# Kernel optimization log

Measured on AMD Instinct MI355X. Metric: run time of the kernel, lower is better.

The kernel has to match this reference:

```python
import jax, jax.numpy as jnp
import numpy as np

MAX_LENGTH = 30
SOS_TOKEN = 2
V, E, H = 32000, 512, 512
B, S = 64, 128


def setup_inputs() -> dict:
    key = jax.random.key(0)
    ks = jax.random.split(key, 16)
    sc = 0.02
    return {
        "encoder_outputs": jax.random.normal(ks[0], (B, S, 2 * H), jnp.float32),
        "encoder_hidden": jax.random.normal(ks[1], (B, H), jnp.float32),
        "target_tensor": jax.random.randint(ks[2], (B, MAX_LENGTH), 0, V, jnp.int32),
        "embedding": jax.random.normal(ks[3], (V, E), jnp.float32) * sc,
        "wa": jax.random.normal(ks[4], (H, H), jnp.float32) * sc,
        "ua": jax.random.normal(ks[5], (H, 2 * H), jnp.float32) * sc,
        "va": jax.random.normal(ks[6], (1, H), jnp.float32) * sc,
        "w_ih": jax.random.normal(ks[7], (3 * H, E + 2 * H), jnp.float32) * sc,
        "w_hh": jax.random.normal(ks[8], (3 * H, H), jnp.float32) * sc,
        "b_ih": jnp.zeros((3 * H,), jnp.float32),
        "b_hh": jnp.zeros((3 * H,), jnp.float32),
        "fc_w": jax.random.normal(ks[9], (V, E + 3 * H), jnp.float32) * sc,
        "fc_b": jnp.zeros((V,), jnp.float32),
    }


def reference(encoder_outputs, encoder_hidden, target_tensor, embedding, wa, ua, va,
              w_ih, w_hh, b_ih, b_hh, fc_w, fc_b):
    b = encoder_outputs.shape[0]
    # teacher-forced input tokens per step: SOS then target[:, :-1]  -> [T, B]
    toks = jnp.concatenate(
        [jnp.full((b, 1), SOS_TOKEN, target_tensor.dtype), target_tensor[:, :-1]], axis=1).T
    enc_ua = jnp.einsum('bsk,hk->bsh', encoder_outputs, ua)  # precompute ua(enc)

    def step(hidden, tok):
        emb = embedding[tok]                                   # [B, E] (dropout = eval mode)
        # Bahdanau attention
        energy = jnp.tanh(hidden @ wa.T[None][0][None][0] if False else jnp.tanh(0))  # placeholder
        energy = jnp.tanh((hidden @ wa.T)[:, None, :] + enc_ua)  # [B, S, H]
        scores = jnp.einsum('bsh,h->bs', energy, va[0])          # [B, S]
        attw = jax.nn.softmax(scores, axis=-1)
        context = jnp.einsum('bs,bsd->bd', attw, encoder_outputs)  # [B, 2H]
        # GRU cell (PyTorch gate order: r, z, n)
        x = jnp.concatenate([emb, context], axis=-1)             # [B, E+2H]
        gi = x @ w_ih.T + b_ih
        gh = hidden @ w_hh.T + b_hh
        i_r, i_z, i_n = jnp.split(gi, 3, axis=-1)
        h_r, h_z, h_n = jnp.split(gh, 3, axis=-1)
        r = jax.nn.sigmoid(i_r + h_r)
        z = jax.nn.sigmoid(i_z + h_z)
        n = jnp.tanh(i_n + r * h_n)
        h_new = (1.0 - z) * n + z * hidden
        out = jnp.concatenate([emb, h_new, context], axis=-1) @ fc_w.T + fc_b  # [B, V]
        return h_new, out

    _, outs = jax.lax.scan(step, encoder_hidden, toks)  # outs: [T, B, V]
    logits = jnp.transpose(outs, (1, 0, 2))             # [B, T, V]
    return jax.nn.log_softmax(logits, axis=-1)
```

## Files before the change

### kernel.cpp

```cpp
#include <hip/hip_runtime.h>

#define B_ 64
#define S_ 128
#define H_ 512
#define E_ 512
#define V_ 32000
#define T_ 30
#define KX_ 1536
#define KF_ 2048

typedef float f32x4 __attribute__((ext_vector_type(4)));
typedef short s16x8 __attribute__((ext_vector_type(8)));
typedef short s16x4 __attribute__((ext_vector_type(4)));

__device__ __forceinline__ short f2bf(float f) {
  union { float f; unsigned u; } v; v.f = f;
  unsigned r = v.u + 0x7fffu + ((v.u >> 16) & 1u);
  return (short)(r >> 16);
}
__device__ __forceinline__ float bf2f(short s) {
  union { unsigned u; float f; } v; v.u = ((unsigned)(unsigned short)s) << 16;
  return v.f;
}

__device__ __forceinline__ f32x4 mfma16(s16x8 a, s16x8 b, f32x4 c) {
  return __builtin_amdgcn_mfma_f32_16x16x32_bf16(a, b, c, 0, 0, 0);
}

__global__ __launch_bounds__(256) void cvt_bf16_kernel(const float* __restrict__ src,
                                                       short* __restrict__ dst, int n4) {
  int i = blockIdx.x * 256 + threadIdx.x;
  if (i >= n4) return;
  f32x4 v = *(const f32x4*)(src + (size_t)i * 4);
  s16x4 o;
  o[0] = f2bf(v[0]); o[1] = f2bf(v[1]); o[2] = f2bf(v[2]); o[3] = f2bf(v[3]);
  *(s16x4*)(dst + (size_t)i * 4) = o;
}

__global__ __launch_bounds__(256) void init_kernel(const float* __restrict__ ehid,
                                                   float* __restrict__ hidden,
                                                   short* __restrict__ xg) {
  int i = blockIdx.x * 256 + threadIdx.x;
  float h = ehid[i];
  hidden[i] = h;
  int b = i >> 9, hh = i & 511;
  xg[b * 2048 + 1536 + hh] = f2bf(h);
}

__global__ __launch_bounds__(256) void enc_ua_kernel(const float* __restrict__ enc,
                                                     const float* __restrict__ ua,
                                                     short* __restrict__ enc_ua) {
  __shared__ short alds[64 * 264];
  int tid = threadIdx.x;
  int wv = tid >> 6, lane = tid & 63;
  int q = lane >> 4, ml = lane & 15;
  int m0 = blockIdx.x * 64;
  int n0 = blockIdx.y * 128 + wv * 32;
  f32x4 acc[4][2];
  f32x4 zz = {0.f, 0.f, 0.f, 0.f};
#pragma unroll
  for (int a = 0; a < 4; a++) { acc[a][0] = zz; acc[a][1] = zz; }

  for (int kc = 0; kc < 4; kc++) {
    __syncthreads();
    for (int i = tid; i < 4096; i += 256) {
      int m = i >> 6, kk = (i & 63) << 2;
      f32x4 v = *(const f32x4*)(enc + (size_t)(m0 + m) * 1024 + kc * 256 + kk);
      s16x4 o;
      o[0] = f2bf(v[0]); o[1] = f2bf(v[1]); o[2] = f2bf(v[2]); o[3] = f2bf(v[3]);
      *(s16x4*)(&alds[m * 264 + kk]) = o;
    }
    __syncthreads();
#pragma unroll
    for (int kt = 0; kt < 8; kt++) {
      int k = kt * 32 + q * 8;
      int gk = kc * 256 + k;
      s16x8 bf[2];
#pragma unroll
      for (int nf = 0; nf < 2; nf++) {
        const float* bp = ua + (size_t)(n0 + nf * 16 + ml) * 1024 + gk;
        f32x4 b0 = *(const f32x4*)bp, b1 = *(const f32x4*)(bp + 4);
        s16x8 t;
        t[0] = f2bf(b0[0]); t[1] = f2bf(b0[1]); t[2] = f2bf(b0[2]); t[3] = f2bf(b0[3]);
        t[4] = f2bf(b1[0]); t[5] = f2bf(b1[1]); t[6] = f2bf(b1[2]); t[7] = f2bf(b1[3]);
        bf[nf] = t;
      }
#pragma unroll
      for (int mt = 0; mt < 4; mt++) {
        s16x8 af = *(const s16x8*)(&alds[(mt * 16 + ml) * 264 + k]);
        acc[mt][0] = mfma16(af, bf[0], acc[mt][0]);
        acc[mt][1] = mfma16(af, bf[1], acc[mt][1]);
      }
    }
  }
#pragma unroll
  for (int nf = 0; nf < 2; nf++) {
    int n = n0 + nf * 16 + ml;
#pragma unroll
    for (int mt = 0; mt < 4; mt++)
#pragma unroll
      for (int r = 0; r < 4; r++) {
        int m = m0 + mt * 16 + q * 4 + r;
        enc_ua[(size_t)m * 512 + n] = f2bf(acc[mt][nf][r]);
      }
  }
}

__global__ __launch_bounds__(256) void prep_kernel(const short* __restrict__ xg_h,
                                                   const short* __restrict__ wab,
                                                   float* __restrict__ qv,
                                                   const float* __restrict__ embedding,
                                                   const int* __restrict__ target,
                                                   short* __restrict__ xg,
                                                   short* __restrict__ xf, int t) {
  int tid = threadIdx.x;
  int wv = tid >> 6, lane = tid & 63;
  int q = lane >> 4, ml = lane & 15;
  int n = blockIdx.x * 64 + wv * 16 + ml;
  f32x4 acc[4];
  f32x4 zz = {0.f, 0.f, 0.f, 0.f};
#pragma unroll
  for (int a = 0; a < 4; a++) acc[a] = zz;

#pragma unroll
  for (int kt = 0; kt < 16; kt++) {
    int k = kt * 32 + q * 8;
    s16x8 bfrag = *(const s16x8*)(wab + (size_t)n * 512 + k);
#pragma unroll
    for (int mt = 0; mt < 4; mt++) {
      s16x8 af = *(const s16x8*)(xg_h + (size_t)(mt * 16 + ml) * 2048 + 1536 + k);
      acc[mt] = mfma16(af, bfrag, acc[mt]);
    }
  }
#pragma unroll
  for (int mt = 0; mt < 4; mt++)
#pragma unroll
    for (int r = 0; r < 4; r++) {
      int b = mt * 16 + q * 4 + r;
      qv[(size_t)b * 512 + n] = acc[mt][r];
    }

  int gid = blockIdx.x * 256 + tid;
#pragma unroll
  for (int it = 0; it < 16; it++) {
    int i = gid + it * 2048;
    int b = i >> 9, h = i & 511;
    int tok = (t == 0) ? 2 : target[b * 30 + (t - 1)];
    short s = f2bf(embedding[(size_t)tok * 512 + h]);
    xg[b * 2048 + h] = s;
    xf[b * 2048 + h] = s;
  }
}

__global__ __launch_bounds__(256) void score_kernel(const float* __restrict__ qv,
                                                    const float* __restrict__ va,
                                                    const short* __restrict__ enc_ua,
                                                    float* __restrict__ scores) {
  int b = blockIdx.x >> 3;
  int sg = blockIdx.x & 7;
  int tid = threadIdx.x;
  int wv = tid >> 6, lane = tid & 63;
  __shared__ float qv_s[512];
  __shared__ float va_s[512];
  for (int i = tid; i < 512; i += 256) {
    qv_s[i] = qv[b * 512 + i];
    va_s[i] = va[i];
  }
  __syncthreads();
#pragma unroll
  for (int r = 0; r < 4; r++) {
    int s = sg * 16 + wv * 4 + r;
    const short* eu = enc_ua + ((size_t)b * 128 + s) * 512 + lane * 8;
    s16x8 e8 = *(const s16x8*)eu;
    float a = 0.f;
#pragma unroll
    for (int j = 0; j < 8; j++) {
      int h = lane * 8 + j;
      float e = qv_s[h] + bf2f(e8[j]);
      float ex = __expf(2.f * e);
      float th = 1.f - 2.f / (ex + 1.f);
      a += th * va_s[h];
    }
#pragma unroll
    for (int off = 32; off > 0; off >>= 1) a += __shfl_down(a, off);
    if (lane == 0) scores[b * 128 + s] = a;
  }
}

template <bool ENCB>
__global__ __launch_bounds__(256) void ctx_kernel(const float* __restrict__ scores,
                                                  const float* __restrict__ encf,
                                                  const short* __restrict__ encb,
                                                  short* __restrict__ xg,
                                                  short* __restrict__ xf) {
  int b = blockIdx.x, tid = threadIdx.x;
  __shared__ float p[128];
  __shared__ float red[128];
  if (tid < 128) { p[tid] = scores[b * 128 + tid]; red[tid] = p[tid]; }
  __syncthreads();
  for (int st = 64; st >= 1; st >>= 1) {
    if (tid < st) red[tid] = fmaxf(red[tid], red[tid + st]);
    __syncthreads();
  }
  float mx = red[0];
  __syncthreads();
  if (tid < 128) { float e = __expf(p[tid] - mx); p[tid] = e; red[tid] = e; }
  __syncthreads();
  for (int st = 64; st >= 1; st >>= 1) {
    if (tid < st) red[tid] += red[tid + st];
    __syncthreads();
  }
  float inv = 1.f / red[0];
  __syncthreads();
  if (tid < 128) p[tid] *= inv;
  __syncthreads();

  int d = blockIdx.y * 256 + tid;
  float a = 0.f;
  if (ENCB) {
    const short* ep = encb + (size_t)b * 128 * 1024 + d;
#pragma unroll 4
    for (int s = 0; s < 128; s++) a += p[s] * bf2f(ep[(size_t)s * 1024]);
  } else {
    const float* ep = encf + (size_t)b * 128 * 1024 + d;
#pragma unroll 4
    for (int s = 0; s < 128; s++) a += p[s] * ep[(size_t)s * 1024];
  }
  short c = f2bf(a);
  xg[b * 2048 + 512 + d] = c;
  xf[b * 2048 + 1024 + d] = c;
}

__global__ __launch_bounds__(256) void gru_gemm_kernel(const short* __restrict__ xg,
                                                       const short* __restrict__ wihb,
                                                       const short* __restrict__ whhb,
                                                       float* __restrict__ gi,
                                                       float* __restrict__ gh) {
  int tid = threadIdx.x;
  int wv = tid >> 6, lane = tid & 63;
  int q = lane >> 4, ml = lane & 15;
  int n = blockIdx.x * 64 + wv * 16 + ml;
  f32x4 acci[4], acch[4];
  f32x4 zz = {0.f, 0.f, 0.f, 0.f};
#pragma unroll
  for (int a = 0; a < 4; a++) { acci[a] = zz; acch[a] = zz; }

  for (int kt = 0; kt < 48; kt++) {
    int k = kt * 32 + q * 8;
    s16x8 bfrag = *(const s16x8*)(wihb + (size_t)n * 1536 + k);
#pragma unroll
    for (int mt = 0; mt < 4; mt++) {
      s16x8 af = *(const s16x8*)(xg + (size_t)(mt * 16 + ml) * 2048 + k);
      acci[mt] = mfma16(af, bfrag, acci[mt]);
    }
  }
  for (int kt = 0; kt < 16; kt++) {
    int k = kt * 32 + q * 8;
    s16x8 bfrag = *(const s16x8*)(whhb + (size_t)n * 512 + k);
#pragma unroll
    for (int mt = 0; mt < 4; mt++) {
      s16x8 af = *(const s16x8*)(xg + (size_t)(mt * 16 + ml) * 2048 + 1536 + k);
      acch[mt] = mfma16(af, bfrag, acch[mt]);
    }
  }
#pragma unroll
  for (int mt = 0; mt < 4; mt++)
#pragma unroll
    for (int r = 0; r < 4; r++) {
      int b = mt * 16 + q * 4 + r;
      gi[(size_t)b * 1536 + n] = acci[mt][r];
      gh[(size_t)b * 1536 + n] = acch[mt][r];
    }
}

__global__ __launch_bounds__(256) void gates_kernel(const float* __restrict__ gi,
                                                    const float* __restrict__ gh,
                                                    const float* __restrict__ bih,
                                                    const float* __restrict__ bhh,
                                                    float* __restrict__ hidden,
                                                    short* __restrict__ xg,
                                                    short* __restrict__ xf) {
  int i = blockIdx.x * 256 + threadIdx.x;
  int b = i >> 9, h = i & 511;
  const float* gib = gi + (size_t)b * 1536;
  const float* ghb = gh + (size_t)b * 1536;
  float ir = gib[h] + bih[h];
  float iz = gib[512 + h] + bih[512 + h];
  float in_ = gib[1024 + h] + bih[1024 + h];
  float hr = ghb[h] + bhh[h];
  float hz = ghb[512 + h] + bhh[512 + h];
  float hn = ghb[1024 + h] + bhh[1024 + h];
  float r = 1.f / (1.f + __expf(-(ir + hr)));
  float z = 1.f / (1.f + __expf(-(iz + hz)));
  float nx = in_ + r * hn;
  float ex = __expf(2.f * nx);
  float n = 1.f - 2.f / (ex + 1.f);
  float hnew = (1.f - z) * n + z * hidden[i];
  hidden[i] = hnew;
  short hb = f2bf(hnew);
  xg[b * 2048 + 1536 + h] = hb;
  xf[b * 2048 + 512 + h] = hb;
}

template <bool PRE>
__global__ __launch_bounds__(256) void fc_kernel(const short* __restrict__ xf,
                                                 const short* __restrict__ fcwb,
                                                 const float* __restrict__ fcwf,
                                                 const float* __restrict__ fcb,
                                                 float* __restrict__ out, int t) {
  __shared__ short alds[64 * 264];
  int tid = threadIdx.x;
  int wv = tid >> 6, lane = tid & 63;
  int q = lane >> 4, ml = lane & 15;
  int n0 = blockIdx.x * 128 + wv * 32;
  f32x4 acc[4][2];
  f32x4 zz = {0.f, 0.f, 0.f, 0.f};
#pragma unroll
  for (int a = 0; a < 4; a++) { acc[a][0] = zz; acc[a][1] = zz; }

  for (int kc = 0; kc < 8; kc++) {
    __syncthreads();
    for (int i = tid; i < 2048; i += 256) {
      int m = i >> 5, kk = (i & 31) << 3;
      *(s16x8*)(&alds[m * 264 + kk]) = *(const s16x8*)(xf + (size_t)m * 2048 + kc * 256 + kk);
    }
    __syncthreads();
#pragma unroll
    for (int kt = 0; kt < 8; kt++) {
      int k = kt * 32 + q * 8;
      int gk = kc * 256 + k;
      s16x8 bf0, bf1;
      if (PRE) {
        bf0 = *(const s16x8*)(fcwb + (size_t)(n0 + ml) * 2048 + gk);
        bf1 = *(const s16x8*)(fcwb + (size_t)(n0 + 16 + ml) * 2048 + gk);
      } else {
        const float* p0 = fcwf + (size_t)(n0 + ml) * 2048 + gk;
        const float* p1 = fcwf + (size_t)(n0 + 16 + ml) * 2048 + gk;
        f32x4 a0 = *(const f32x4*)p0, a1 = *(const f32x4*)(p0 + 4);
        f32x4 b0 = *(const f32x4*)p1, b1 = *(const f32x4*)(p1 + 4);
        bf0[0] = f2bf(a0[0]); bf0[1] = f2bf(a0[1]); bf0[2] = f2bf(a0[2]); bf0[3] = f2bf(a0[3]);
        bf0[4] = f2bf(a1[0]); bf0[5] = f2bf(a1[1]); bf0[6] = f2bf(a1[2]); bf0[7] = f2bf(a1[3]);
        bf1[0] = f2bf(b0[0]); bf1[1] = f2bf(b0[1]); bf1[2] = f2bf(b0[2]); bf1[3] = f2bf(b0[3]);
        bf1[4] = f2bf(b1[0]); bf1[5] = f2bf(b1[1]); bf1[6] = f2bf(b1[2]); bf1[7] = f2bf(b1[3]);
      }
#pragma unroll
      for (int mt = 0; mt < 4; mt++) {
        s16x8 af = *(const s16x8*)(&alds[(mt * 16 + ml) * 264 + k]);
        acc[mt][0] = mfma16(af, bf0, acc[mt][0]);
        acc[mt][1] = mfma16(af, bf1, acc[mt][1]);
      }
    }
  }
#pragma unroll
  for (int nf = 0; nf < 2; nf++) {
    int v = n0 + nf * 16 + ml;
    float bias = fcb[v];
#pragma unroll
    for (int mt = 0; mt < 4; mt++)
#pragma unroll
      for (int r = 0; r < 4; r++) {
        int b = mt * 16 + q * 4 + r;
        out[((size_t)b * T_ + t) * V_ + v] = acc[mt][nf][r] + bias;
      }
  }
}

__global__ __launch_bounds__(256) void finalize_kernel(float* __restrict__ out, int t) {
  int b = blockIdx.x, tid = threadIdx.x;
  float* row = out + ((size_t)b * T_ + t) * V_;
  __shared__ float red[256];
  float mx = -3.4e38f;
  for (int i = tid; i < 8000; i += 256) {
    f32x4 v = *(const f32x4*)(row + i * 4);
    mx = fmaxf(mx, fmaxf(fmaxf(v[0], v[1]), fmaxf(v[2], v[3])));
  }
  red[tid] = mx; __syncthreads();
  for (int st = 128; st >= 1; st >>= 1) {
    if (tid < st) red[tid] = fmaxf(red[tid], red[tid + st]);
    __syncthreads();
  }
  mx = red[0]; __syncthreads();
  float sm = 0.f;
  for (int i = tid; i < 8000; i += 256) {
    f32x4 v = *(const f32x4*)(row + i * 4);
    sm += __expf(v[0] - mx) + __expf(v[1] - mx) + __expf(v[2] - mx) + __expf(v[3] - mx);
  }
  red[tid] = sm; __syncthreads();
  for (int st = 128; st >= 1; st >>= 1) {
    if (tid < st) red[tid] += red[tid + st];
    __syncthreads();
  }
  float lse = mx + __logf(red[0]);
  for (int i = tid; i < 8000; i += 256) {
    f32x4 v = *(const f32x4*)(row + i * 4);
    v[0] -= lse; v[1] -= lse; v[2] -= lse; v[3] -= lse;
    *(f32x4*)(row + i * 4) = v;
  }
}

extern "C" void kernel_launch(void* const* d_in, const int* in_sizes, int n_in,
                              void* d_out, int out_size, void* d_ws, size_t ws_size,
                              hipStream_t stream) {
  const float* enc  = (const float*)d_in[0];
  const float* ehid = (const float*)d_in[1];
  const int*   tgt  = (const int*)  d_in[2];
  const float* emb  = (const float*)d_in[3];
  const float* wa   = (const float*)d_in[4];
  const float* ua   = (const float*)d_in[5];
  const float* va   = (const float*)d_in[6];
  const float* wih  = (const float*)d_in[7];
  const float* whh  = (const float*)d_in[8];
  const float* bih  = (const float*)d_in[9];
  const float* bhh  = (const float*)d_in[10];
  const float* fcw  = (const float*)d_in[11];
  const float* fcb  = (const float*)d_in[12];
  float* out = (float*)d_out;

  const size_t SZ_FCWB = (size_t)V_ * KF_ * 2;
  const size_t SZ_ENCB = (size_t)B_ * S_ * 1024 * 2;
  char* ws = (char*)d_ws;
  size_t off = 0;
  auto take = [&](size_t bytes) -> char* {
    char* p = ws + off;
    off = (off + bytes + 255) & ~(size_t)255;
    return p;
  };
  size_t small_need;
  {
    size_t o = 0;
    auto sim = [&](size_t bb) { o = (o + bb + 255) & ~(size_t)255; };
    sim((size_t)B_ * S_ * H_ * 2);
    sim((size_t)3 * H_ * KX_ * 2);
    sim((size_t)3 * H_ * H_ * 2);
    sim((size_t)H_ * H_ * 2);
    sim((size_t)B_ * H_ * 4);
    sim((size_t)B_ * H_ * 4);
    sim((size_t)B_ * S_ * 4);
    sim((size_t)B_ * KF_ * 2);
    sim((size_t)B_ * KF_ * 2);
    sim((size_t)B_ * 3 * H_ * 4);
    sim((size_t)B_ * 3 * H_ * 4);
    small_need = o;
  }
  bool PRE  = ws_size >= SZ_FCWB + small_need + 512;
  bool ENCB = ws_size >= SZ_FCWB + SZ_ENCB + small_need + 1024;

  short* fcwb = PRE ? (short*)take(SZ_FCWB) : nullptr;
  short* encb = ENCB ? (short*)take(SZ_ENCB) : nullptr;
  short* enc_ua = (short*)take((size_t)B_ * S_ * H_ * 2);
  short* wihb   = (short*)take((size_t)3 * H_ * KX_ * 2);
  short* whhb   = (short*)take((size_t)3 * H_ * H_ * 2);
  short* wab    = (short*)take((size_t)H_ * H_ * 2);
  float* hidden = (float*)take((size_t)B_ * H_ * 4);
  float* qv     = (float*)take((size_t)B_ * H_ * 4);
  float* scores = (float*)take((size_t)B_ * S_ * 4);
  short* xg     = (short*)take((size_t)B_ * KF_ * 2);
  short* xf     = (short*)take((size_t)B_ * KF_ * 2);
  float* gi     = (float*)take((size_t)B_ * 3 * H_ * 4);
  float* gh     = (float*)take((size_t)B_ * 3 * H_ * 4);

  if (PRE)
    cvt_bf16_kernel<<<(V_ * KF_ / 4 + 255) / 256, 256, 0, stream>>>(fcw, fcwb, V_ * KF_ / 4);
  if (ENCB)
    cvt_bf16_kernel<<<(B_ * S_ * 1024 / 4 + 255) / 256, 256, 0, stream>>>(enc, encb, B_ * S_ * 1024 / 4);
  cvt_bf16_kernel<<<(3 * H_ * KX_ / 4 + 255) / 256, 256, 0, stream>>>(wih, wihb, 3 * H_ * KX_ / 4);
  cvt_bf16_kernel<<<(3 * H_ * H_ / 4 + 255) / 256, 256, 0, stream>>>(whh, whhb, 3 * H_ * H_ / 4);
  cvt_bf16_kernel<<<(H_ * H_ / 4 + 255) / 256, 256, 0, stream>>>(wa, wab, H_ * H_ / 4);
  init_kernel<<<(B_ * H_) / 256, 256, 0, stream>>>(ehid, hidden, xg);
  enc_ua_kernel<<<dim3(128, 4), 256, 0, stream>>>(enc, ua, enc_ua);

  for (int t = 0; t < T_; t++) {
    prep_kernel<<<8, 256, 0, stream>>>(xg, wab, qv, emb, tgt, xg, xf, t);
    score_kernel<<<B_ * 8, 256, 0, stream>>>(qv, va, enc_ua, scores);
    if (ENCB)
      ctx_kernel<true><<<dim3(B_, 4), 256, 0, stream>>>(scores, enc, encb, xg, xf);
    else
      ctx_kernel<false><<<dim3(B_, 4), 256, 0, stream>>>(scores, enc, encb, xg, xf);
    gru_gemm_kernel<<<24, 256, 0, stream>>>(xg, wihb, whhb, gi, gh);
    gates_kernel<<<(B_ * H_) / 256, 256, 0, stream>>>(gi, gh, bih, bhh, hidden, xg, xf);
    if (PRE)
      fc_kernel<true><<<V_ / 128, 256, 0, stream>>>(xf, fcwb, fcw, fcb, out, t);
    else
      fc_kernel<false><<<V_ / 128, 256, 0, stream>>>(xf, fcwb, fcw, fcb, out, t);
    finalize_kernel<<<B_, 256, 0, stream>>>(out, t);
  }
}
```

Baseline: 4.705 ms.

## Replace per-step kernel launches with a persistent decoder kernel using grid barriers

```diff
diff --git a/kernel.cpp b/kernel.cpp
--- a/kernel.cpp
+++ b/kernel.cpp
@@ -22,9 +22,19 @@
   union { unsigned u; float f; } v; v.u = ((unsigned)(unsigned short)s) << 16;
   return v.f;
 }
-
 __device__ __forceinline__ f32x4 mfma16(s16x8 a, s16x8 b, f32x4 c) {
   return __builtin_amdgcn_mfma_f32_16x16x32_bf16(a, b, c, 0, 0, 0);
+}
+
+__device__ __forceinline__ void gbar(unsigned* cnt, unsigned target) {
+  __threadfence();
+  __syncthreads();
+  if (threadIdx.x == 0) {
+    atomicAdd(cnt, 1u);
+    while (atomicAdd(cnt, 0u) < target) __builtin_amdgcn_s_sleep(1);
+  }
+  __syncthreads();
+  __threadfence();
 }
 
 __global__ __launch_bounds__(256) void cvt_bf16_kernel(const float* __restrict__ src,
@@ -39,8 +49,10 @@
 
 __global__ __launch_bounds__(256) void init_kernel(const float* __restrict__ ehid,
                                                    float* __restrict__ hidden,
-                                                   short* __restrict__ xg) {
+                                                   short* __restrict__ xg,
+                                                   unsigned* __restrict__ bar) {
   int i = blockIdx.x * 256 + threadIdx.x;
+  if (blockIdx.x == 0 && threadIdx.x < 64) bar[threadIdx.x] = 0u;
   float h = ehid[i];
   hidden[i] = h;
   int b = i >> 9, hh = i & 511;
@@ -80,10 +92,10 @@
       for (int nf = 0; nf < 2; nf++) {
         const float* bp = ua + (size_t)(n0 + nf * 16 + ml) * 1024 + gk;
         f32x4 b0 = *(const f32x4*)bp, b1 = *(const f32x4*)(bp + 4);
-        s16x8 t;
-        t[0] = f2bf(b0[0]); t[1] = f2bf(b0[1]); t[2] = f2bf(b0[2]); t[3] = f2bf(b0[3]);
-        t[4] = f2bf(b1[0]); t[5] = f2bf(b1[1]); t[6] = f2bf(b1[2]); t[7] = f2bf(b1[3]);
-        bf[nf] = t;
+        s16x8 tt;
+        tt[0] = f2bf(b0[0]); tt[1] = f2bf(b0[1]); tt[2] = f2bf(b0[2]); tt[3] = f2bf(b0[3]);
+        tt[4] = f2bf(b1[0]); tt[5] = f2bf(b1[1]); tt[6] = f2bf(b1[2]); tt[7] = f2bf(b1[3]);
+        bf[nf] = tt;
       }
 #pragma unroll
       for (int mt = 0; mt < 4; mt++) {
@@ -106,272 +118,83 @@
   }
 }
 
-__global__ __launch_bounds__(256) void prep_kernel(const short* __restrict__ xg_h,
-                                                   const short* __restrict__ wab,
-                                                   float* __restrict__ qv,
-                                                   const float* __restrict__ embedding,
-                                                   const int* __restrict__ target,
-                                                   short* __restrict__ xg,
-                                                   short* __restrict__ xf, int t) {
-  int tid = threadIdx.x;
-  int wv = tid >> 6, lane = tid & 63;
-  int q = lane >> 4, ml = lane & 15;
-  int n = blockIdx.x * 64 + wv * 16 + ml;
+__global__ __launch_bounds__(256) void emb_gather_kernel(const float* __restrict__ emb,
+                                                         const int* __restrict__ tgt,
+                                                         short* __restrict__ emb_all) {
+  int b = blockIdx.x, t = blockIdx.y, tid = threadIdx.x;
+  int tok = (t == 0) ? 2 : tgt[b * 30 + (t - 1)];
+  const float* src = emb + (size_t)tok * 512;
+  short* dst = emb_all + ((size_t)t * 64 + b) * 512;
+  int h = tid * 2;
+  float a0 = src[h], a1 = src[h + 1];
+  dst[h] = f2bf(a0); dst[h + 1] = f2bf(a1);
+}
+
+struct PP {
+  const short* fcwb; const float* fcwf; const float* fcb;
+  const short* encb; const float* encf;
+  const short* enc_ua; const short* wab;
+  const short* wihb; const short* whhb;
+  const float* bih; const float* bhh; const float* va;
+  const short* emb_all;
+  short* xg0; short* xg1; short* xf0; short* xf1;
+  float* hid0; float* hid1; float* qv; float* out;
+  unsigned* bar;
+};
+
+template <bool PRE>
+static __device__ void fc_tile(int tile, int tf, const short* __restrict__ xfb,
+                               const PP& P, float* smf) {
+  short* alds = (short*)smf;
+  const int tid = threadIdx.x;
+  const int wv = tid >> 6, lane = tid & 63;
+  const int q = lane >> 4, ml = lane & 15;
+  const int n = tile * 64 + wv * 16 + ml;
+  const f32x4 zz = {0.f, 0.f, 0.f, 0.f};
   f32x4 acc[4];
-  f32x4 zz = {0.f, 0.f, 0.f, 0.f};
-#pragma unroll
-  for (int a = 0; a < 4; a++) acc[a] = zz;
-
-#pragma unroll
-  for (int kt = 0; kt < 16; kt++) {
-    int k = kt * 32 + q * 8;
-    s16x8 bfrag = *(const s16x8*)(wab + (size_t)n * 512 + k);
-#pragma unroll
-    for (int mt = 0; mt < 4; mt++) {
-      s16x8 af = *(const s16x8*)(xg_h + (size_t)(mt * 16 + ml) * 2048 + 1536 + k);
-      acc[mt] = mfma16(af, bfrag, acc[mt]);
-    }
-  }
-#pragma unroll
-  for (int mt = 0; mt < 4; mt++)
-#pragma unroll
-    for (int r = 0; r < 4; r++) {
-      int b = mt * 16 + q * 4 + r;
-      qv[(size_t)b * 512 + n] = acc[mt][r];
-    }
-
-  int gid = blockIdx.x * 256 + tid;
-#pragma unroll
-  for (int it = 0; it < 16; it++) {
-    int i = gid + it * 2048;
-    int b = i >> 9, h = i & 511;
-    int tok = (t == 0) ? 2 : target[b * 30 + (t - 1)];
-    short s = f2bf(embedding[(size_t)tok * 512 + h]);
-    xg[b * 2048 + h] = s;
-    xf[b * 2048 + h] = s;
-  }
-}
-
-__global__ __launch_bounds__(256) void score_kernel(const float* __restrict__ qv,
-                                                    const float* __restrict__ va,
-                                                    const short* __restrict__ enc_ua,
-                                                    float* __restrict__ scores) {
-  int b = blockIdx.x >> 3;
-  int sg = blockIdx.x & 7;
-  int tid = threadIdx.x;
-  int wv = tid >> 6, lane = tid & 63;
-  __shared__ float qv_s[512];
-  __shared__ float va_s[512];
-  for (int i = tid; i < 512; i += 256) {
-    qv_s[i] = qv[b * 512 + i];
-    va_s[i] = va[i];
-  }
-  __syncthreads();
-#pragma unroll
-  for (int r = 0; r < 4; r++) {
-    int s = sg * 16 + wv * 4 + r;
-    const short* eu = enc_ua + ((size_t)b * 128 + s) * 512 + lane * 8;
-    s16x8 e8 = *(const s16x8*)eu;
-    float a = 0.f;
-#pragma unroll
-    for (int j = 0; j < 8; j++) {
-      int h = lane * 8 + j;
-      float e = qv_s[h] + bf2f(e8[j]);
-      float ex = __expf(2.f * e);
-      float th = 1.f - 2.f / (ex + 1.f);
-      a += th * va_s[h];
-    }
-#pragma unroll
-    for (int off = 32; off > 0; off >>= 1) a += __shfl_down(a, off);
-    if (lane == 0) scores[b * 128 + s] = a;
-  }
-}
-
-template <bool ENCB>
-__global__ __launch_bounds__(256) void ctx_kernel(const float* __restrict__ scores,
-                                                  const float* __restrict__ encf,
-                                                  const short* __restrict__ encb,
-                                                  short* __restrict__ xg,
-                                                  short* __restrict__ xf) {
-  int b = blockIdx.x, tid = threadIdx.x;
-  __shared__ float p[128];
-  __shared__ float red[128];
-  if (tid < 128) { p[tid] = scores[b * 128 + tid]; red[tid] = p[tid]; }
-  __syncthreads();
-  for (int st = 64; st >= 1; st >>= 1) {
-    if (tid < st) red[tid] = fmaxf(red[tid], red[tid + st]);
-    __syncthreads();
-  }
-  float mx = red[0];
-  __syncthreads();
-  if (tid < 128) { float e = __expf(p[tid] - mx); p[tid] = e; red[tid] = e; }
-  __syncthreads();
-  for (int st = 64; st >= 1; st >>= 1) {
-    if (tid < st) red[tid] += red[tid + st];
-    __syncthreads();
-  }
-  float inv = 1.f / red[0];
-  __syncthreads();
-  if (tid < 128) p[tid] *= inv;
-  __syncthreads();
-
-  int d = blockIdx.y * 256 + tid;
-  float a = 0.f;
-  if (ENCB) {
-    const short* ep = encb + (size_t)b * 128 * 1024 + d;
-#pragma unroll 4
-    for (int s = 0; s < 128; s++) a += p[s] * bf2f(ep[(size_t)s * 1024]);
-  } else {
-    const float* ep = encf + (size_t)b * 128 * 1024 + d;
-#pragma unroll 4
-    for (int s = 0; s < 128; s++) a += p[s] * ep[(size_t)s * 1024];
-  }
-  short c = f2bf(a);
-  xg[b * 2048 + 512 + d] = c;
-  xf[b * 2048 + 1024 + d] = c;
-}
-
-__global__ __launch_bounds__(256) void gru_gemm_kernel(const short* __restrict__ xg,
-                                                       const short* __restrict__ wihb,
-                                                       const short* __restrict__ whhb,
-                                                       float* __restrict__ gi,
-                                                       float* __restrict__ gh) {
-  int tid = threadIdx.x;
-  int wv = tid >> 6, lane = tid & 63;
-  int q = lane >> 4, ml = lane & 15;
-  int n = blockIdx.x * 64 + wv * 16 + ml;
-  f32x4 acci[4], acch[4];
-  f32x4 zz = {0.f, 0.f, 0.f, 0.f};
-#pragma unroll
-  for (int a = 0; a < 4; a++) { acci[a] = zz; acch[a] = zz; }
-
-  for (int kt = 0; kt < 48; kt++) {
-    int k = kt * 32 + q * 8;
-    s16x8 bfrag = *(const s16x8*)(wihb + (size_t)n * 1536 + k);
-#pragma unroll
-    for (int mt = 0; mt < 4; mt++) {
-      s16x8 af = *(const s16x8*)(xg + (size_t)(mt * 16 + ml) * 2048 + k);
-      acci[mt] = mfma16(af, bfrag, acci[mt]);
-    }
-  }
-  for (int kt = 0; kt < 16; kt++) {
-    int k = kt * 32 + q * 8;
-    s16x8 bfrag = *(const s16x8*)(whhb + (size_t)n * 512 + k);
-#pragma unroll
-    for (int mt = 0; mt < 4; mt++) {
-      s16x8 af = *(const s16x8*)(xg + (size_t)(mt * 16 + ml) * 2048 + 1536 + k);
-      acch[mt] = mfma16(af, bfrag, acch[mt]);
-    }
-  }
-#pragma unroll
-  for (int mt = 0; mt < 4; mt++)
-#pragma unroll
-    for (int r = 0; r < 4; r++) {
-      int b = mt * 16 + q * 4 + r;
-      gi[(size_t)b * 1536 + n] = acci[mt][r];
-      gh[(size_t)b * 1536 + n] = acch[mt][r];
-    }
-}
-
-__global__ __launch_bounds__(256) void gates_kernel(const float* __restrict__ gi,
-                                                    const float* __restrict__ gh,
-                                                    const float* __restrict__ bih,
-                                                    const float* __restrict__ bhh,
-                                                    float* __restrict__ hidden,
-                                                    short* __restrict__ xg,
-                                                    short* __restrict__ xf) {
-  int i = blockIdx.x * 256 + threadIdx.x;
-  int b = i >> 9, h = i & 511;
-  const float* gib = gi + (size_t)b * 1536;
-  const float* ghb = gh + (size_t)b * 1536;
-  float ir = gib[h] + bih[h];
-  float iz = gib[512 + h] + bih[512 + h];
-  float in_ = gib[1024 + h] + bih[1024 + h];
-  float hr = ghb[h] + bhh[h];
-  float hz = ghb[512 + h] + bhh[512 + h];
-  float hn = ghb[1024 + h] + bhh[1024 + h];
-  float r = 1.f / (1.f + __expf(-(ir + hr)));
-  float z = 1.f / (1.f + __expf(-(iz + hz)));
-  float nx = in_ + r * hn;
-  float ex = __expf(2.f * nx);
-  float n = 1.f - 2.f / (ex + 1.f);
-  float hnew = (1.f - z) * n + z * hidden[i];
-  hidden[i] = hnew;
-  short hb = f2bf(hnew);
-  xg[b * 2048 + 1536 + h] = hb;
-  xf[b * 2048 + 512 + h] = hb;
-}
-
-template <bool PRE>
-__global__ __launch_bounds__(256) void fc_kernel(const short* __restrict__ xf,
-                                                 const short* __restrict__ fcwb,
-                                                 const float* __restrict__ fcwf,
-                                                 const float* __restrict__ fcb,
-                                                 float* __restrict__ out, int t) {
-  __shared__ short alds[64 * 264];
-  int tid = threadIdx.x;
-  int wv = tid >> 6, lane = tid & 63;
-  int q = lane >> 4, ml = lane & 15;
-  int n0 = blockIdx.x * 128 + wv * 32;
-  f32x4 acc[4][2];
-  f32x4 zz = {0.f, 0.f, 0.f, 0.f};
-#pragma unroll
-  for (int a = 0; a < 4; a++) { acc[a][0] = zz; acc[a][1] = zz; }
-
+  acc[0] = zz; acc[1] = zz; acc[2] = zz; acc[3] = zz;
   for (int kc = 0; kc < 8; kc++) {
     __syncthreads();
     for (int i = tid; i < 2048; i += 256) {
       int m = i >> 5, kk = (i & 31) << 3;
-      *(s16x8*)(&alds[m * 264 + kk]) = *(const s16x8*)(xf + (size_t)m * 2048 + kc * 256 + kk);
+      *(s16x8*)(&alds[m * 264 + kk]) = *(const s16x8*)(xfb + (size_t)m * 2048 + kc * 256 + kk);
     }
     __syncthreads();
 #pragma unroll
     for (int kt = 0; kt < 8; kt++) {
       int k = kt * 32 + q * 8;
       int gk = kc * 256 + k;
-      s16x8 bf0, bf1;
+      s16x8 bf;
       if (PRE) {
-        bf0 = *(const s16x8*)(fcwb + (size_t)(n0 + ml) * 2048 + gk);
-        bf1 = *(const s16x8*)(fcwb + (size_t)(n0 + 16 + ml) * 2048 + gk);
+        bf = *(const s16x8*)(P.fcwb + (size_t)n * 2048 + gk);
       } else {
-        const float* p0 = fcwf + (size_t)(n0 + ml) * 2048 + gk;
-        const float* p1 = fcwf + (size_t)(n0 + 16 + ml) * 2048 + gk;
+        const float* p0 = P.fcwf + (size_t)n * 2048 + gk;
         f32x4 a0 = *(const f32x4*)p0, a1 = *(const f32x4*)(p0 + 4);
-        f32x4 b0 = *(const f32x4*)p1, b1 = *(const f32x4*)(p1 + 4);
-        bf0[0] = f2bf(a0[0]); bf0[1] = f2bf(a0[1]); bf0[2] = f2bf(a0[2]); bf0[3] = f2bf(a0[3]);
-        bf0[4] = f2bf(a1[0]); bf0[5] = f2bf(a1[1]); bf0[6] = f2bf(a1[2]); bf0[7] = f2bf(a1[3]);
-        bf1[0] = f2bf(b0[0]); bf1[1] = f2bf(b0[1]); bf1[2] = f2bf(b0[2]); bf1[3] = f2bf(b0[3]);
-        bf1[4] = f2bf(b1[0]); bf1[5] = f2bf(b1[1]); bf1[6] = f2bf(b1[2]); bf1[7] = f2bf(b1[3]);
+        bf[0] = f2bf(a0[0]); bf[1] = f2bf(a0[1]); bf[2] = f2bf(a0[2]); bf[3] = f2bf(a0[3]);
+        bf[4] = f2bf(a1[0]); bf[5] = f2bf(a1[1]); bf[6] = f2bf(a1[2]); bf[7] = f2bf(a1[3]);
       }
 #pragma unroll
       for (int mt = 0; mt < 4; mt++) {
         s16x8 af = *(const s16x8*)(&alds[(mt * 16 + ml) * 264 + k]);
-        acc[mt][0] = mfma16(af, bf0, acc[mt][0]);
-        acc[mt][1] = mfma16(af, bf1, acc[mt][1]);
-      }
-    }
-  }
-#pragma unroll
-  for (int nf = 0; nf < 2; nf++) {
-    int v = n0 + nf * 16 + ml;
-    float bias = fcb[v];
-#pragma unroll
-    for (int mt = 0; mt < 4; mt++)
-#pragma unroll
-      for (int r = 0; r < 4; r++) {
-        int b = mt * 16 + q * 4 + r;
-        out[((size_t)b * T_ + t) * V_ + v] = acc[mt][nf][r] + bias;
-      }
-  }
-}
-
-__global__ __launch_bounds__(256) void finalize_kernel(float* __restrict__ out, int t) {
-  int b = blockIdx.x, tid = threadIdx.x;
-  float* row = out + ((size_t)b * T_ + t) * V_;
-  __shared__ float red[256];
+        acc[mt] = mfma16(af, bf, acc[mt]);
+      }
+    }
+  }
+  float bias = P.fcb[n];
+#pragma unroll
+  for (int mt = 0; mt < 4; mt++)
+#pragma unroll
+    for (int r = 0; r < 4; r++) {
+      int b = mt * 16 + q * 4 + r;
+      P.out[((size_t)b * T_ + tf) * V_ + n] = acc[mt][r] + bias;
+    }
+}
+
+static __device__ void finalize_row(float* __restrict__ row, float* red) {
+  const int tid = threadIdx.x;
   float mx = -3.4e38f;
   for (int i = tid; i < 8000; i += 256) {
-    f32x4 v = *(const f32x4*)(row + i * 4);
+    f32x4 v = *(const f32x4*)(row + (size_t)i * 4);
     mx = fmaxf(mx, fmaxf(fmaxf(v[0], v[1]), fmaxf(v[2], v[3])));
   }
   red[tid] = mx; __syncthreads();
@@ -382,7 +205,7 @@
   mx = red[0]; __syncthreads();
   float sm = 0.f;
   for (int i = tid; i < 8000; i += 256) {
-    f32x4 v = *(const f32x4*)(row + i * 4);
+    f32x4 v = *(const f32x4*)(row + (size_t)i * 4);
     sm += __expf(v[0] - mx) + __expf(v[1] - mx) + __expf(v[2] - mx) + __expf(v[3] - mx);
   }
   red[tid] = sm; __syncthreads();
@@ -392,9 +215,230 @@
   }
   float lse = mx + __logf(red[0]);
   for (int i = tid; i < 8000; i += 256) {
-    f32x4 v = *(const f32x4*)(row + i * 4);
+    f32x4 v = *(const f32x4*)(row + (size_t)i * 4);
     v[0] -= lse; v[1] -= lse; v[2] -= lse; v[3] -= lse;
-    *(f32x4*)(row + i * 4) = v;
+    *(f32x4*)(row + (size_t)i * 4) = v;
+  }
+}
+
+template <bool ENCB>
+static __device__ void attn_block(int b, short* __restrict__ xg_cur, short* __restrict__ xf_cur,
+                                  const PP& P, float* smf) {
+  float* q_s = smf; float* va_s = smf + 512; float* p_s = smf + 1024; float* red = smf + 1152;
+  const int tid = threadIdx.x;
+  const int wv = tid >> 6, lane = tid & 63;
+  for (int i = tid; i < 512; i += 256) {
+    q_s[i] = P.qv[(size_t)b * 512 + i];
+    va_s[i] = P.va[i];
+  }
+  __syncthreads();
+  float qr[8], vr[8];
+#pragma unroll
+  for (int j = 0; j < 8; j++) { qr[j] = q_s[lane * 8 + j]; vr[j] = va_s[lane * 8 + j]; }
+  for (int r = 0; r < 32; r++) {
+    int s = wv * 32 + r;
+    s16x8 e8 = *(const s16x8*)(P.enc_ua + ((size_t)b * 128 + s) * 512 + lane * 8);
+    float a = 0.f;
+#pragma unroll
+    for (int j = 0; j < 8; j++) {
+      float e = qr[j] + bf2f(e8[j]);
+      float ex = __expf(2.f * e);
+      a += (1.f - 2.f / (ex + 1.f)) * vr[j];
+    }
+#pragma unroll
+    for (int off = 32; off > 0; off >>= 1) a += __shfl_down(a, off);
+    if (lane == 0) p_s[s] = a;
+  }
+  __syncthreads();
+  if (tid < 128) red[tid] = p_s[tid];
+  __syncthreads();
+  for (int st = 64; st >= 1; st >>= 1) {
+    if (tid < st) red[tid] = fmaxf(red[tid], red[tid + st]);
+    __syncthreads();
+  }
+  float mx = red[0]; __syncthreads();
+  if (tid < 128) { float e = __expf(p_s[tid] - mx); p_s[tid] = e; red[tid] = e; }
+  __syncthreads();
+  for (int st = 64; st >= 1; st >>= 1) {
+    if (tid < st) red[tid] += red[tid + st];
+    __syncthreads();
+  }
+  float inv = 1.f / red[0]; __syncthreads();
+  if (tid < 128) p_s[tid] *= inv;
+  __syncthreads();
+  int d4 = tid * 4;
+  f32x4 a = {0.f, 0.f, 0.f, 0.f};
+  if (ENCB) {
+    const short* ep = P.encb + (size_t)b * 128 * 1024 + d4;
+#pragma unroll 4
+    for (int s = 0; s < 128; s++) {
+      s16x4 e = *(const s16x4*)(ep + (size_t)s * 1024);
+      float p = p_s[s];
+      a[0] += p * bf2f(e[0]); a[1] += p * bf2f(e[1]);
+      a[2] += p * bf2f(e[2]); a[3] += p * bf2f(e[3]);
+    }
+  } else {
+    const float* ep = P.encf + (size_t)b * 128 * 1024 + d4;
+#pragma unroll 4
+    for (int s = 0; s < 128; s++) {
+      f32x4 e = *(const f32x4*)(ep + (size_t)s * 1024);
+      float p = p_s[s];
+      a[0] += p * e[0]; a[1] += p * e[1]; a[2] += p * e[2]; a[3] += p * e[3];
+    }
+  }
+  s16x4 c4;
+  c4[0] = f2bf(a[0]); c4[1] = f2bf(a[1]); c4[2] = f2bf(a[2]); c4[3] = f2bf(a[3]);
+  *(s16x4*)(xg_cur + (size_t)b * 2048 + 512 + d4) = c4;
+  *(s16x4*)(xf_cur + (size_t)b * 2048 + 1024 + d4) = c4;
+}
+
+static __device__ void gru_block(int bid, const short* __restrict__ xg_cur,
+                                 short* __restrict__ xg_nxt, short* __restrict__ xf_cur,
+                                 const float* __restrict__ hid_cur, float* __restrict__ hid_nxt,
+                                 const PP& P, float* gsm) {
+  const int tid = threadIdx.x;
+  const int wv = tid >> 6, lane = tid & 63;
+  const int q = lane >> 4, ml = lane & 15;
+  const int c16 = bid * 16;
+  const int c = c16 + ml;
+  const f32x4 zz = {0.f, 0.f, 0.f, 0.f};
+  f32x4 acc[3][4];
+#pragma unroll
+  for (int g = 0; g < 3; g++)
+#pragma unroll
+    for (int mt = 0; mt < 4; mt++) acc[g][mt] = zz;
+
+  if (wv < 3) {
+    const int kbase = wv * 512;
+    for (int kt = 0; kt < 16; kt++) {
+      int k = kbase + kt * 32 + q * 8;
+      s16x8 af[4];
+#pragma unroll
+      for (int mt = 0; mt < 4; mt++)
+        af[mt] = *(const s16x8*)(xg_cur + (size_t)(mt * 16 + ml) * 2048 + k);
+#pragma unroll
+      for (int g = 0; g < 3; g++) {
+        s16x8 bf = *(const s16x8*)(P.wihb + (size_t)(g * 512 + c) * 1536 + k);
+#pragma unroll
+        for (int mt = 0; mt < 4; mt++) acc[g][mt] = mfma16(af[mt], bf, acc[g][mt]);
+      }
+    }
+  } else {
+    for (int kt = 0; kt < 16; kt++) {
+      int k = kt * 32 + q * 8;
+      s16x8 af[4];
+#pragma unroll
+      for (int mt = 0; mt < 4; mt++)
+        af[mt] = *(const s16x8*)(xg_cur + (size_t)(mt * 16 + ml) * 2048 + 1536 + k);
+#pragma unroll
+      for (int g = 0; g < 3; g++) {
+        s16x8 bf = *(const s16x8*)(P.whhb + (size_t)(g * 512 + c) * 512 + k);
+#pragma unroll
+        for (int mt = 0; mt < 4; mt++) acc[g][mt] = mfma16(af[mt], bf, acc[g][mt]);
+      }
+    }
+  }
+#pragma unroll
+  for (int g = 0; g < 3; g++)
+#pragma unroll
+    for (int mt = 0; mt < 4; mt++)
+#pragma unroll
+      for (int r = 0; r < 4; r++)
+        gsm[((wv * 3 + g) * 64 + mt * 16 + q * 4 + r) * 17 + ml] = acc[g][mt][r];
+  __syncthreads();
+#pragma unroll
+  for (int j = 0; j < 4; j++) {
+    int o = tid + j * 256;
+    int cc = o & 15, bb = o >> 4;
+    int hcol = c16 + cc;
+    float gi0 = gsm[((0) * 64 + bb) * 17 + cc] + gsm[((3) * 64 + bb) * 17 + cc] + gsm[((6) * 64 + bb) * 17 + cc];
+    float gi1 = gsm[((1) * 64 + bb) * 17 + cc] + gsm[((4) * 64 + bb) * 17 + cc] + gsm[((7) * 64 + bb) * 17 + cc];
+    float gi2 = gsm[((2) * 64 + bb) * 17 + cc] + gsm[((5) * 64 + bb) * 17 + cc] + gsm[((8) * 64 + bb) * 17 + cc];
+    float gh0 = gsm[((9) * 64 + bb) * 17 + cc];
+    float gh1 = gsm[((10) * 64 + bb) * 17 + cc];
+    float gh2 = gsm[((11) * 64 + bb) * 17 + cc];
+    float ir = gi0 + P.bih[hcol],         hr = gh0 + P.bhh[hcol];
+    float iz = gi1 + P.bih[512 + hcol],   hz = gh1 + P.bhh[512 + hcol];
+    float in_ = gi2 + P.bih[1024 + hcol], hn = gh2 + P.bhh[1024 + hcol];
+    float r = 1.f / (1.f + __expf(-(ir + hr)));
+    float z = 1.f / (1.f + __expf(-(iz + hz)));
+    float nx = in_ + r * hn;
+    float ex = __expf(2.f * nx);
+    float n = 1.f - 2.f / (ex + 1.f);
+    float hold = hid_cur[(size_t)bb * 512 + hcol];
+    float hnew = (1.f - z) * n + z * hold;
+    hid_nxt[(size_t)bb * 512 + hcol] = hnew;
+    short hb = f2bf(hnew);
+    xg_nxt[(size_t)bb * 2048 + 1536 + hcol] = hb;
+    xf_cur[(size_t)bb * 2048 + 512 + hcol] = hb;
+  }
+}
+
+template <bool PRE, bool ENCB>
+__global__ __launch_bounds__(256) void decoder_persist(PP P) {
+  __shared__ __align__(16) float sm[13872];
+  const int bid = blockIdx.x, tid = threadIdx.x;
+  const int wv = tid >> 6, lane = tid & 63;
+  const int q = lane >> 4, ml = lane & 15;
+  const f32x4 zz = {0.f, 0.f, 0.f, 0.f};
+  unsigned nb = 0;
+
+  for (int t = 0; t < T_ + 2; t++) {
+    short* xg_cur = (t & 1) ? P.xg1 : P.xg0;
+    short* xg_nxt = (t & 1) ? P.xg0 : P.xg1;
+    short* xf_cur = (t & 1) ? P.xf1 : P.xf0;
+    const short* xf_prev = (t & 1) ? P.xf0 : P.xf1;
+    const float* hid_cur = (t & 1) ? P.hid1 : P.hid0;
+    float* hid_nxt = (t & 1) ? P.hid0 : P.hid1;
+
+    if (t < T_ && bid < 8) {
+      int n = bid * 64 + wv * 16 + ml;
+      f32x4 acc[4];
+      acc[0] = zz; acc[1] = zz; acc[2] = zz; acc[3] = zz;
+#pragma unroll
+      for (int kt = 0; kt < 16; kt++) {
+        int k = kt * 32 + q * 8;
+        s16x8 bfrag = *(const s16x8*)(P.wab + (size_t)n * 512 + k);
+#pragma unroll
+        for (int mt = 0; mt < 4; mt++) {
+          s16x8 af = *(const s16x8*)(xg_cur + (size_t)(mt * 16 + ml) * 2048 + 1536 + k);
+          acc[mt] = mfma16(af, bfrag, acc[mt]);
+        }
+      }
+#pragma unroll
+      for (int mt = 0; mt < 4; mt++)
+#pragma unroll
+        for (int r = 0; r < 4; r++)
+          P.qv[(size_t)(mt * 16 + q * 4 + r) * 512 + n] = acc[mt][r];
+      int gid = bid * 256 + tid;
+      int idx = gid * 16;
+      int b2 = idx >> 9, hh = idx & 511;
+      const s16x8* src = (const s16x8*)(P.emb_all + (size_t)t * 32768 + idx);
+      s16x8 e0 = src[0], e1 = src[1];
+      *(s16x8*)(xg_cur + (size_t)b2 * 2048 + hh) = e0;
+      *(s16x8*)(xg_cur + (size_t)b2 * 2048 + hh + 8) = e1;
+      *(s16x8*)(xf_cur + (size_t)b2 * 2048 + hh) = e0;
+      *(s16x8*)(xf_cur + (size_t)b2 * 2048 + hh + 8) = e1;
+    } else if (t >= 2 && bid >= 8 && bid < 72) {
+      finalize_row(P.out + ((size_t)(bid - 8) * T_ + (t - 2)) * V_, sm);
+    } else if (t >= 1 && t <= T_ && bid >= 72 && bid < 239) {
+      fc_tile<PRE>(bid - 72, t - 1, xf_prev, P, sm);
+    }
+    gbar(P.bar, ++nb * 256u);
+
+    if (t < T_ && bid < 64) {
+      attn_block<ENCB>(bid, xg_cur, xf_cur, P, sm);
+    } else if (t >= 1 && t <= T_ && bid >= 64 && bid < 231) {
+      fc_tile<PRE>(167 + bid - 64, t - 1, xf_prev, P, sm);
+    }
+    gbar(P.bar, ++nb * 256u);
+
+    if (t < T_ && bid < 32) {
+      gru_block(bid, xg_cur, xg_nxt, xf_cur, hid_cur, hid_nxt, P, sm);
+    } else if (t >= 1 && t <= T_ && bid >= 32 && bid < 198) {
+      fc_tile<PRE>(334 + bid - 32, t - 1, xf_prev, P, sm);
+    }
+    gbar(P.bar, ++nb * 256u);
   }
 }
 
@@ -433,13 +477,15 @@
     sim((size_t)3 * H_ * KX_ * 2);
     sim((size_t)3 * H_ * H_ * 2);
     sim((size_t)H_ * H_ * 2);
+    sim((size_t)T_ * B_ * H_ * 2);
+    sim((size_t)B_ * KF_ * 2);
+    sim((size_t)B_ * KF_ * 2);
+    sim((size_t)B_ * KF_ * 2);
+    sim((size_t)B_ * KF_ * 2);
     sim((size_t)B_ * H_ * 4);
     sim((size_t)B_ * H_ * 4);
-    sim((size_t)B_ * S_ * 4);
-    sim((size_t)B_ * KF_ * 2);
-    sim((size_t)B_ * KF_ * 2);
-    sim((size_t)B_ * 3 * H_ * 4);
-    sim((size_t)B_ * 3 * H_ * 4);
+    sim((size_t)B_ * H_ * 4);
+    sim(256);
     small_need = o;
   }
   bool PRE  = ws_size >= SZ_FCWB + small_need + 512;
@@ -447,17 +493,19 @@
 
   short* fcwb = PRE ? (short*)take(SZ_FCWB) : nullptr;
   short* encb = ENCB ? (short*)take(SZ_ENCB) : nullptr;
-  short* enc_ua = (short*)take((size_t)B_ * S_ * H_ * 2);
-  short* wihb   = (short*)take((size_t)3 * H_ * KX_ * 2);
-  short* whhb   = (short*)take((size_t)3 * H_ * H_ * 2);
-  short* wab    = (short*)take((size_t)H_ * H_ * 2);
-  float* hidden = (float*)take((size_t)B_ * H_ * 4);
-  float* qv     = (float*)take((size_t)B_ * H_ * 4);
-  float* scores = (float*)take((size_t)B_ * S_ * 4);
-  short* xg     = (short*)take((size_t)B_ * KF_ * 2);
-  short* xf     = (short*)take((size_t)B_ * KF_ * 2);
-  float* gi     = (float*)take((size_t)B_ * 3 * H_ * 4);
-  float* gh     = (float*)take((size_t)B_ * 3 * H_ * 4);
+  short* enc_ua  = (short*)take((size_t)B_ * S_ * H_ * 2);
+  short* wihb    = (short*)take((size_t)3 * H_ * KX_ * 2);
+  short* whhb    = (short*)take((size_t)3 * H_ * H_ * 2);
+  short* wab     = (short*)take((size_t)H_ * H_ * 2);
+  short* emb_all = (short*)take((size_t)T_ * B_ * H_ * 2);
+  short* xg0     = (short*)take((size_t)B_ * KF_ * 2);
+  short* xg1     = (short*)take((size_t)B_ * KF_ * 2);
+  short* xf0     = (short*)take((size_t)B_ * KF_ * 2);
+  short* xf1     = (short*)take((size_t)B_ * KF_ * 2);
+  float* hid0    = (float*)take((size_t)B_ * H_ * 4);
+  float* hid1    = (float*)take((size_t)B_ * H_ * 4);
+  float* qv      = (float*)take((size_t)B_ * H_ * 4);
+  unsigned* bar  = (unsigned*)take(256);
 
   if (PRE)
     cvt_bf16_kernel<<<(V_ * KF_ / 4 + 255) / 256, 256, 0, stream>>>(fcw, fcwb, V_ * KF_ / 4);
@@ -466,22 +514,22 @@
   cvt_bf16_kernel<<<(3 * H_ * KX_ / 4 + 255) / 256, 256, 0, stream>>>(wih, wihb, 3 * H_ * KX_ / 4);
   cvt_bf16_kernel<<<(3 * H_ * H_ / 4 + 255) / 256, 256, 0, stream>>>(whh, whhb, 3 * H_ * H_ / 4);
   cvt_bf16_kernel<<<(H_ * H_ / 4 + 255) / 256, 256, 0, stream>>>(wa, wab, H_ * H_ / 4);
-  init_kernel<<<(B_ * H_) / 256, 256, 0, stream>>>(ehid, hidden, xg);
+  init_kernel<<<(B_ * H_) / 256, 256, 0, stream>>>(ehid, hid0, xg0, bar);
   enc_ua_kernel<<<dim3(128, 4), 256, 0, stream>>>(enc, ua, enc_ua);
-
-  for (int t = 0; t < T_; t++) {
-    prep_kernel<<<8, 256, 0, stream>>>(xg, wab, qv, emb, tgt, xg, xf, t);
-    score_kernel<<<B_ * 8, 256, 0, stream>>>(qv, va, enc_ua, scores);
-    if (ENCB)
-      ctx_kernel<true><<<dim3(B_, 4), 256, 0, stream>>>(scores, enc, encb, xg, xf);
-    else
-      ctx_kernel<false><<<dim3(B_, 4), 256, 0, stream>>>(scores, enc, encb, xg, xf);
-    gru_gemm_kernel<<<24, 256, 0, stream>>>(xg, wihb, whhb, gi, gh);
-    gates_kernel<<<(B_ * H_) / 256, 256, 0, stream>>>(gi, gh, bih, bhh, hidden, xg, xf);
-    if (PRE)
-      fc_kernel<true><<<V_ / 128, 256, 0, stream>>>(xf, fcwb, fcw, fcb, out, t);
-    else
-      fc_kernel<false><<<V_ / 128, 256, 0, stream>>>(xf, fcwb, fcw, fcb, out, t);
-    finalize_kernel<<<B_, 256, 0, stream>>>(out, t);
-  }
-}
+  emb_gather_kernel<<<dim3(B_, T_), 256, 0, stream>>>(emb, tgt, emb_all);
+
+  PP p;
+  p.fcwb = fcwb; p.fcwf = fcw; p.fcb = fcb;
+  p.encb = encb; p.encf = enc;
+  p.enc_ua = enc_ua; p.wab = wab; p.wihb = wihb; p.whhb = whhb;
+  p.bih = bih; p.bhh = bhh; p.va = va;
+  p.emb_all = emb_all;
+  p.xg0 = xg0; p.xg1 = xg1; p.xf0 = xf0; p.xf1 = xf1;
+  p.hid0 = hid0; p.hid1 = hid1; p.qv = qv; p.out = out;
+  p.bar = bar;
+
+  if (PRE && ENCB)      decoder_persist<true, true><<<256, 256, 0, stream>>>(p);
+  else if (PRE)         decoder_persist<true, false><<<256, 256, 0, stream>>>(p);
+  else if (ENCB)        decoder_persist<false, true><<<256, 256, 0, stream>>>(p);
+  else                  decoder_persist<false, false><<<256, 256, 0, stream>>>(p);
+}
```

New measurement: 8.704 ms. 1.85x slower.
